# Kernel optimization log

Measured on AMD Instinct MI355X. Metric: run time of the kernel, lower is better.

The kernel has to match this reference:

```python
import jax, jax.numpy as jnp
import numpy as np


def setup_inputs() -> dict:
    key = jax.random.key(0)
    k1, _ = jax.random.split(key)
    N, H, W, C = 32, 1024, 1024, 2
    inp = jax.random.normal(k1, (N, H, W, C), dtype=jnp.float32)
    theta = jnp.zeros((1,), dtype=jnp.float32)
    return {"input": inp, "theta": theta}


def reference(input, theta):
    # input: [N, H, W, 2] -> NCHW
    x = jnp.transpose(input, (0, 3, 1, 2))
    N, C, H, W = x.shape
    s = 1.0 + theta[0]  # uniform scaling factor (affine = s * identity)

    # torch affine_grid / grid_sample with align_corners=False (default):
    # normalized output coords x_n = (2j+1)/W - 1; sampled coord = s * x_n;
    # pixel coord ix = ((x_n_sampled + 1) * W - 1) / 2. Grid is separable
    # (x depends only on column, y only on row) -> two 1D interpolations.
    xn = (2.0 * jnp.arange(W, dtype=x.dtype) + 1.0) / W - 1.0
    yn = (2.0 * jnp.arange(H, dtype=x.dtype) + 1.0) / H - 1.0
    ix = ((s * xn + 1.0) * W - 1.0) / 2.0  # [W]
    iy = ((s * yn + 1.0) * H - 1.0) / 2.0  # [H]

    def corners(coord, size):
        c0 = jnp.floor(coord)
        c1 = c0 + 1.0
        w1 = coord - c0
        w0 = 1.0 - w1
        # zeros padding: out-of-range corners contribute 0
        m0 = ((c0 >= 0) & (c0 <= size - 1)).astype(coord.dtype)
        m1 = ((c1 >= 0) & (c1 <= size - 1)).astype(coord.dtype)
        i0 = jnp.clip(c0, 0, size - 1).astype(jnp.int32)
        i1 = jnp.clip(c1, 0, size - 1).astype(jnp.int32)
        return i0, i1, w0 * m0, w1 * m1

    x0, x1, wx0, wx1 = corners(ix, W)
    y0, y1, wy0, wy1 = corners(iy, H)

    # interpolate along W (last axis), weights broadcast over [N,C,H,W]
    row = wx0 * x[..., x0] + wx1 * x[..., x1]  # [N, C, H, W]
    # interpolate along H
    out = wy0[:, None] * row[:, :, y0, :] + wy1[:, None] * row[:, :, y1, :]
    return jnp.transpose(out, (0, 2, 3, 1))  # back to NHWC
```

## Files before the change

kernel.cpp:

```cpp
#include <hip/hip_runtime.h>


typedef float f32x4 __attribute__((ext_vector_type(4)));

__global__ __launch_bounds__(256) void ComplexScaling_kernel(
    const float* __restrict__ in, const float* __restrict__ theta,
    float* __restrict__ out, int H, int W) {
  const float s = 1.0f + theta[0];

  const int i = blockIdx.y;
  const int n = blockIdx.z;
  const int j = (blockIdx.x * blockDim.x + threadIdx.x) << 2;
  if (j >= W) return;

  const long long row_elems = (long long)(n * H + i) * W;
  const long long off = (row_elems + j) * 2;

  if (s == 1.0f) {
    const f32x4* __restrict__ src = (const f32x4*)(in + off);
    f32x4* __restrict__ dst = (f32x4*)(out + off);
    f32x4 v0 = __builtin_nontemporal_load(src);
    f32x4 v1 = __builtin_nontemporal_load(src + 1);
    __builtin_nontemporal_store(v0, dst);
    __builtin_nontemporal_store(v1, dst + 1);
    return;
  }

  float yn  = (2.0f * (float)i + 1.0f) / (float)H - 1.0f;
  float iy  = ((s * yn + 1.0f) * (float)H - 1.0f) * 0.5f;
  float fy0 = floorf(iy);
  float wy1 = iy - fy0;
  float wy0 = 1.0f - wy1;
  float fy1 = fy0 + 1.0f;
  float Hm1 = (float)(H - 1);
  if (!(fy0 >= 0.0f && fy0 <= Hm1)) wy0 = 0.0f;
  if (!(fy1 >= 0.0f && fy1 <= Hm1)) wy1 = 0.0f;
  int y0 = (int)fminf(fmaxf(fy0, 0.0f), Hm1);
  int y1 = (int)fminf(fmaxf(fy1, 0.0f), Hm1);

  const float* __restrict__ row0 = in + ((long long)(n * H + y0) * W) * 2;
  const float* __restrict__ row1 = in + ((long long)(n * H + y1) * W) * 2;
  const bool need_y1 = (wy1 != 0.0f);

  float Wm1 = (float)(W - 1);
  float vx[4], vy[4];

  #pragma unroll
  for (int p = 0; p < 4; ++p) {
    int jj = j + p;
    float xn  = (2.0f * (float)jj + 1.0f) / (float)W - 1.0f;
    float ix  = ((s * xn + 1.0f) * (float)W - 1.0f) * 0.5f;
    float fx0 = floorf(ix);
    float wx1 = ix - fx0;
    float wx0 = 1.0f - wx1;
    float fx1 = fx0 + 1.0f;
    if (!(fx0 >= 0.0f && fx0 <= Wm1)) wx0 = 0.0f;
    if (!(fx1 >= 0.0f && fx1 <= Wm1)) wx1 = 0.0f;
    int x0 = (int)fminf(fmaxf(fx0, 0.0f), Wm1);
    int x1 = (int)fminf(fmaxf(fx1, 0.0f), Wm1);

    float ax = 0.0f, ay = 0.0f;
    if (wx0 != 0.0f) {
      const float2 a00 = *(const float2*)(row0 + 2 * x0);
      ax = wx0 * a00.x; ay = wx0 * a00.y;
    }
    if (wx1 != 0.0f) {
      const float2 a01 = *(const float2*)(row0 + 2 * x1);
      ax += wx1 * a01.x; ay += wx1 * a01.y;
    }
    float ox = wy0 * ax, oy = wy0 * ay;

    if (need_y1) {
      float bx = 0.0f, by = 0.0f;
      if (wx0 != 0.0f) {
        const float2 a10 = *(const float2*)(row1 + 2 * x0);
        bx = wx0 * a10.x; by = wx0 * a10.y;
      }
      if (wx1 != 0.0f) {
        const float2 a11 = *(const float2*)(row1 + 2 * x1);
        bx += wx1 * a11.x; by += wx1 * a11.y;
      }
      ox += wy1 * bx; oy += wy1 * by;
    }
    vx[p] = ox; vy[p] = oy;
  }

  f32x4 r0, r1;
  r0.x = vx[0]; r0.y = vy[0]; r0.z = vx[1]; r0.w = vy[1];
  r1.x = vx[2]; r1.y = vy[2]; r1.z = vx[3]; r1.w = vy[3];

  f32x4* __restrict__ dst = (f32x4*)(out + off);
  __builtin_nontemporal_store(r0, dst);
  __builtin_nontemporal_store(r1, dst + 1);
}

extern "C" void kernel_launch(void* const* d_in, const int* in_sizes, int n_in,
                              void* d_out, int out_size, void* d_ws, size_t ws_size,
                              hipStream_t stream) {
  const float* in    = (const float*)d_in[0];
  const float* theta = (const float*)d_in[1];
  float* out = (float*)d_out;

  const int N = 32, H = 1024, W = 1024;
  dim3 block(256, 1, 1);
  dim3 grid((W + 1023) / 1024, H, N);
  ComplexScaling_kernel<<<grid, block, 0, stream>>>(in, theta, out, H, W);
}
```

Measured before the change: 458.0 us.

## Switch to grid-stride persistent loop with 16-byte per-thread vectors

```diff
diff --git a/kernel.cpp b/kernel.cpp
--- a/kernel.cpp
+++ b/kernel.cpp
@@ -5,93 +5,92 @@
 
 __global__ __launch_bounds__(256) void ComplexScaling_kernel(
     const float* __restrict__ in, const float* __restrict__ theta,
-    float* __restrict__ out, int H, int W) {
+    float* __restrict__ out) {
+  constexpr int H = 1024, W = 1024;
+  constexpr int NVEC = 16777216;
   const float s = 1.0f + theta[0];
 
-  const int i = blockIdx.y;
-  const int n = blockIdx.z;
-  const int j = (blockIdx.x * blockDim.x + threadIdx.x) << 2;
-  if (j >= W) return;
-
-  const long long row_elems = (long long)(n * H + i) * W;
-  const long long off = (row_elems + j) * 2;
+  const int tid0 = blockIdx.x * blockDim.x + threadIdx.x;
+  const int nthreads = gridDim.x * blockDim.x;
 
   if (s == 1.0f) {
-    const f32x4* __restrict__ src = (const f32x4*)(in + off);
-    f32x4* __restrict__ dst = (f32x4*)(out + off);
-    f32x4 v0 = __builtin_nontemporal_load(src);
-    f32x4 v1 = __builtin_nontemporal_load(src + 1);
-    __builtin_nontemporal_store(v0, dst);
-    __builtin_nontemporal_store(v1, dst + 1);
+    const f32x4* __restrict__ src = (const f32x4*)in;
+    f32x4* __restrict__ dst = (f32x4*)out;
+    #pragma unroll 4
+    for (int v = tid0; v < NVEC; v += nthreads) {
+      dst[v] = src[v];
+    }
     return;
   }
 
-  float yn  = (2.0f * (float)i + 1.0f) / (float)H - 1.0f;
-  float iy  = ((s * yn + 1.0f) * (float)H - 1.0f) * 0.5f;
-  float fy0 = floorf(iy);
-  float wy1 = iy - fy0;
-  float wy0 = 1.0f - wy1;
-  float fy1 = fy0 + 1.0f;
-  float Hm1 = (float)(H - 1);
-  if (!(fy0 >= 0.0f && fy0 <= Hm1)) wy0 = 0.0f;
-  if (!(fy1 >= 0.0f && fy1 <= Hm1)) wy1 = 0.0f;
-  int y0 = (int)fminf(fmaxf(fy0, 0.0f), Hm1);
-  int y1 = (int)fminf(fmaxf(fy1, 0.0f), Hm1);
+  const float Hm1 = (float)(H - 1);
+  const float Wm1 = (float)(W - 1);
 
-  const float* __restrict__ row0 = in + ((long long)(n * H + y0) * W) * 2;
-  const float* __restrict__ row1 = in + ((long long)(n * H + y1) * W) * 2;
-  const bool need_y1 = (wy1 != 0.0f);
+  for (int v = tid0; v < NVEC; v += nthreads) {
+    const int j = (v & (W / 2 - 1)) << 1;
+    const int i = (v >> 9) & (H - 1);
+    const int n = v >> 19;
 
-  float Wm1 = (float)(W - 1);
-  float vx[4], vy[4];
+    float yn  = (2.0f * (float)i + 1.0f) / (float)H - 1.0f;
+    float iy  = ((s * yn + 1.0f) * (float)H - 1.0f) * 0.5f;
+    float fy0 = floorf(iy);
+    float wy1 = iy - fy0;
+    float wy0 = 1.0f - wy1;
+    float fy1 = fy0 + 1.0f;
+    if (!(fy0 >= 0.0f && fy0 <= Hm1)) wy0 = 0.0f;
+    if (!(fy1 >= 0.0f && fy1 <= Hm1)) wy1 = 0.0f;
+    int y0 = (int)fminf(fmaxf(fy0, 0.0f), Hm1);
+    int y1 = (int)fminf(fmaxf(fy1, 0.0f), Hm1);
 
-  #pragma unroll
-  for (int p = 0; p < 4; ++p) {
-    int jj = j + p;
-    float xn  = (2.0f * (float)jj + 1.0f) / (float)W - 1.0f;
-    float ix  = ((s * xn + 1.0f) * (float)W - 1.0f) * 0.5f;
-    float fx0 = floorf(ix);
-    float wx1 = ix - fx0;
-    float wx0 = 1.0f - wx1;
-    float fx1 = fx0 + 1.0f;
-    if (!(fx0 >= 0.0f && fx0 <= Wm1)) wx0 = 0.0f;
-    if (!(fx1 >= 0.0f && fx1 <= Wm1)) wx1 = 0.0f;
-    int x0 = (int)fminf(fmaxf(fx0, 0.0f), Wm1);
-    int x1 = (int)fminf(fmaxf(fx1, 0.0f), Wm1);
+    const float* __restrict__ row0 = in + ((long long)(n * H + y0) * W) * 2;
+    const float* __restrict__ row1 = in + ((long long)(n * H + y1) * W) * 2;
+    const bool need_y1 = (wy1 != 0.0f);
 
-    float ax = 0.0f, ay = 0.0f;
-    if (wx0 != 0.0f) {
-      const float2 a00 = *(const float2*)(row0 + 2 * x0);
-      ax = wx0 * a00.x; ay = wx0 * a00.y;
-    }
-    if (wx1 != 0.0f) {
-      const float2 a01 = *(const float2*)(row0 + 2 * x1);
-      ax += wx1 * a01.x; ay += wx1 * a01.y;
-    }
-    float ox = wy0 * ax, oy = wy0 * ay;
+    float vx[2], vy[2];
+    #pragma unroll
+    for (int p = 0; p < 2; ++p) {
+      int jj = j + p;
+      float xn  = (2.0f * (float)jj + 1.0f) / (float)W - 1.0f;
+      float ix  = ((s * xn + 1.0f) * (float)W - 1.0f) * 0.5f;
+      float fx0 = floorf(ix);
+      float wx1 = ix - fx0;
+      float wx0 = 1.0f - wx1;
+      float fx1 = fx0 + 1.0f;
+      if (!(fx0 >= 0.0f && fx0 <= Wm1)) wx0 = 0.0f;
+      if (!(fx1 >= 0.0f && fx1 <= Wm1)) wx1 = 0.0f;
+      int x0 = (int)fminf(fmaxf(fx0, 0.0f), Wm1);
+      int x1 = (int)fminf(fmaxf(fx1, 0.0f), Wm1);
 
-    if (need_y1) {
-      float bx = 0.0f, by = 0.0f;
+      float ax = 0.0f, ay = 0.0f;
       if (wx0 != 0.0f) {
-        const float2 a10 = *(const float2*)(row1 + 2 * x0);
-        bx = wx0 * a10.x; by = wx0 * a10.y;
+        const float2 a00 = *(const float2*)(row0 + 2 * x0);
+        ax = wx0 * a00.x; ay = wx0 * a00.y;
       }
       if (wx1 != 0.0f) {
-        const float2 a11 = *(const float2*)(row1 + 2 * x1);
-        bx += wx1 * a11.x; by += wx1 * a11.y;
+        const float2 a01 = *(const float2*)(row0 + 2 * x1);
+        ax += wx1 * a01.x; ay += wx1 * a01.y;
       }
-      ox += wy1 * bx; oy += wy1 * by;
+      float ox = wy0 * ax, oy = wy0 * ay;
+
+      if (need_y1) {
+        float bx = 0.0f, by = 0.0f;
+        if (wx0 != 0.0f) {
+          const float2 a10 = *(const float2*)(row1 + 2 * x0);
+          bx = wx0 * a10.x; by = wx0 * a10.y;
+        }
+        if (wx1 != 0.0f) {
+          const float2 a11 = *(const float2*)(row1 + 2 * x1);
+          bx += wx1 * a11.x; by += wx1 * a11.y;
+        }
+        ox += wy1 * bx; oy += wy1 * by;
+      }
+      vx[p] = ox; vy[p] = oy;
     }
-    vx[p] = ox; vy[p] = oy;
+
+    f32x4 r;
+    r.x = vx[0]; r.y = vy[0]; r.z = vx[1]; r.w = vy[1];
+    ((f32x4*)out)[v] = r;
   }
-
-  f32x4 r0, r1;
-  r0.x = vx[0]; r0.y = vy[0]; r0.z = vx[1]; r0.w = vy[1];
-  r1.x = vx[2]; r1.y = vy[2]; r1.z = vx[3]; r1.w = vy[3];
-
-  f32x4* __restrict__ dst = (f32x4*)(out + off);
-  __builtin_nontemporal_store(r0, dst);
-  __builtin_nontemporal_store(r1, dst + 1);
 }
 
 extern "C" void kernel_launch(void* const* d_in, const int* in_sizes, int n_in,
@@ -101,8 +100,7 @@
   const float* theta = (const float*)d_in[1];
   float* out = (float*)d_out;
 
-  const int N = 32, H = 1024, W = 1024;
   dim3 block(256, 1, 1);
-  dim3 grid((W + 1023) / 1024, H, N);
-  ComplexScaling_kernel<<<grid, block, 0, stream>>>(in, theta, out, H, W);
+  dim3 grid(2048, 1, 1);
+  ComplexScaling_kernel<<<grid, block, 0, stream>>>(in, theta, out);
 }
```

Measured after the change: 456.3 us. No clear change (-0.4%).
